# Optimization experiments

Hardware: AMD Instinct MI355X
Metric: run time of the kernel (lower is better)

## Reference

```python
import jax, jax.numpy as jnp
import numpy as np

N_NODES = 50000
N_EDGES = 800000
IN_F = 256
HEADS = 4
C = 32  # out_features // heads = 128 // 4
OUT_F = HEADS * C
NEG_SLOPE = 0.2
BN_EPS = 1e-5


def setup_inputs() -> dict:
    key = jax.random.key(0)
    ks = jax.random.split(key, 6)
    x = jax.random.normal(ks[0], (N_NODES, IN_F), dtype=jnp.float32)
    edge_index = jax.random.randint(ks[1], (2, N_EDGES), 0, N_NODES, dtype=jnp.int64)
    W = jax.random.normal(ks[2], (IN_F, OUT_F), dtype=jnp.float32) * 0.05
    att_src = jax.random.normal(ks[3], (HEADS, C), dtype=jnp.float32) * 0.05
    att_dst = jax.random.normal(ks[4], (HEADS, C), dtype=jnp.float32) * 0.05
    bias = jnp.zeros((OUT_F,), dtype=jnp.float32)
    gamma = jnp.ones((OUT_F,), dtype=jnp.float32)
    beta = jnp.zeros((OUT_F,), dtype=jnp.float32)
    return {"x": x, "edge_index": edge_index, "W": W, "att_src": att_src,
            "att_dst": att_dst, "bias": bias, "gamma": gamma, "beta": beta}


def reference(x, edge_index, W, att_src, att_dst, bias, gamma, beta):
    N = x.shape[0]
    # PyG GATConv adds self-loops by default
    loops = jnp.arange(N, dtype=edge_index.dtype)
    src = jnp.concatenate([edge_index[0], loops])  # [E+N]
    dst = jnp.concatenate([edge_index[1], loops])  # [E+N]

    h = (x @ W).reshape(N, HEADS, C)               # [N, H, C]
    a_src = jnp.sum(h * att_src, axis=-1)          # [N, H]
    a_dst = jnp.sum(h * att_dst, axis=-1)          # [N, H]

    e = a_src[src] + a_dst[dst]                    # [E', H]
    e = jax.nn.leaky_relu(e, NEG_SLOPE)
    # segment softmax over destination neighborhoods (self-loops ensure no empty segments)
    e_max = jax.ops.segment_max(e, dst, num_segments=N)
    e = jnp.exp(e - e_max[dst])
    denom = jax.ops.segment_sum(e, dst, num_segments=N)
    alpha = e / (denom[dst] + 1e-16)               # [E', H]

    msg = h[src] * alpha[:, :, None]               # [E', H, C]
    out = jax.ops.segment_sum(msg, dst, num_segments=N).reshape(N, OUT_F) + bias

    # BatchNorm1d in training mode (batch statistics, biased variance)
    mean = jnp.mean(out, axis=0)
    var = jnp.var(out, axis=0)
    out = (out - mean) * jax.lax.rsqrt(var + BN_EPS) * gamma + beta
    # ELU; dropout is identity in eval / deterministic reference
    return jax.nn.elu(out)
```

## Files before the change

kernel.cpp:

```cpp
#include <hip/hip_runtime.h>
#include <hip/hip_fp16.h>
#include <math.h>

#define NN 50000
#define EE 800000
#define EP (EE + NN)
#define INF_ 256
#define OF 128
#define NEG_SLOPE 0.2f
#define BN_EPS 1e-5f
#define NB 196
#define NWIN 8
#define DPW 6250
#define NCH 32
#define QPC 6250

typedef _Float16 half8 __attribute__((ext_vector_type(8)));
typedef float floatx4 __attribute__((ext_vector_type(4)));
typedef int intx4 __attribute__((ext_vector_type(4)));

__device__ __forceinline__ float lrelu_exp(float v) {
    v = v > 0.f ? v : NEG_SLOPE * v;
    return expf(v);
}

__global__ __launch_bounds__(256) void k_wprep(const float* __restrict__ W, _Float16* __restrict__ wfrag,
                                               float* __restrict__ fsum)
{
    int idx = blockIdx.x * 256 + threadIdx.x;
    if (idx < 256) fsum[idx] = 0.f;
    int j   = idx & 7;
    int l   = (idx >> 3) & 63;
    int t   = (idx >> 9) & 7;
    int ksg = idx >> 12;
    int k   = ksg * 32 + ((l >> 4) << 3) + j;
    int col = t * 16 + (l & 15);
    wfrag[idx] = (_Float16)W[k * OF + col];
}

__global__ __launch_bounds__(256) void k_gemm(
    const float* __restrict__ x, const _Float16* __restrict__ wfrag,
    const float* __restrict__ att_s, const float* __restrict__ att_d,
    _Float16* __restrict__ h, float* __restrict__ a_src, float* __restrict__ a_dst)
{
    __shared__ __align__(16) _Float16 smem[8192];
    _Float16* xh = smem;

    const int tid  = threadIdx.x;
    const int l    = tid & 63;
    const int w    = tid >> 6;
    const int row0 = blockIdx.x * 64;
    const int lrow = l & 15;
    const int lk8  = (l >> 4) << 3;

    floatx4 acc[8];
    #pragma unroll
    for (int t = 0; t < 8; ++t) acc[t] = (floatx4){0.f, 0.f, 0.f, 0.f};

    for (int kc = 0; kc < 4; ++kc) {
        __syncthreads();
        #pragma unroll
        for (int it = 0; it < 4; ++it) {
            int i  = tid + (it << 8);
            int r  = i >> 4;
            int c4 = (i & 15) << 2;
            int rr = row0 + r; if (rr >= NN) rr = NN - 1;
            float4 v = *(const float4*)&x[rr * INF_ + (kc << 6) + c4];
            _Float16* p = &xh[r * 72 + c4];
            p[0] = (_Float16)v.x; p[1] = (_Float16)v.y;
            p[2] = (_Float16)v.z; p[3] = (_Float16)v.w;
        }
        __syncthreads();
        #pragma unroll
        for (int ks = 0; ks < 2; ++ks) {
            int ksg = kc * 2 + ks;
            half8 a = *(half8*)&xh[(w * 16 + lrow) * 72 + (ks << 5) + lk8];
            const _Float16* wf = &wfrag[(ksg << 12) + (l << 3)];
            #pragma unroll
            for (int t = 0; t < 8; ++t) {
                half8 b = *(const half8*)&wf[t << 9];
                acc[t] = __builtin_amdgcn_mfma_f32_16x16x32_f16(a, b, acc[t], 0, 0, 0);
            }
        }
    }

    float as_c[8], ad_c[8];
    #pragma unroll
    for (int t = 0; t < 8; ++t) { as_c[t] = att_s[t * 16 + lrow]; ad_c[t] = att_d[t * 16 + lrow]; }
    float my_s = 0.f, my_d = 0.f;
    #pragma unroll
    for (int hh = 0; hh < 4; ++hh) {
        #pragma unroll
        for (int reg = 0; reg < 4; ++reg) {
            float ps = acc[2*hh][reg] * as_c[2*hh] + acc[2*hh+1][reg] * as_c[2*hh+1];
            float pd = acc[2*hh][reg] * ad_c[2*hh] + acc[2*hh+1][reg] * ad_c[2*hh+1];
            ps += __shfl_xor(ps, 1); ps += __shfl_xor(ps, 2); ps += __shfl_xor(ps, 4); ps += __shfl_xor(ps, 8);
            pd += __shfl_xor(pd, 1); pd += __shfl_xor(pd, 2); pd += __shfl_xor(pd, 4); pd += __shfl_xor(pd, 8);
            if (lrow == hh * 4 + reg) { my_s = ps; my_d = pd; }
        }
    }
    {
        int myreg = lrow & 3, myhh = lrow >> 2;
        int myrow = row0 + w * 16 + ((l >> 4) << 2) + myreg;
        if (myrow < NN) { a_src[myrow * 4 + myhh] = my_s; a_dst[myrow * 4 + myhh] = my_d; }
    }

    __syncthreads();
    _Float16* ldso = smem + w * 2048;
    #pragma unroll
    for (int t = 0; t < 8; ++t)
        #pragma unroll
        for (int reg = 0; reg < 4; ++reg)
            ldso[(((l >> 4) << 2) + reg) * 128 + t * 16 + lrow] = (_Float16)acc[t][reg];
    __syncthreads();
    {
        _Float16* gdst = h + (size_t)(row0 + w * 16) * OF;
        #pragma unroll
        for (int q = 0; q < 4; ++q) {
            int off = (q << 9) + (l << 3);
            *(half8*)&gdst[off] = *(half8*)&ldso[off];
        }
    }
}

__global__ __launch_bounds__(1024) void k_winhist(const int* __restrict__ ei, int* __restrict__ counts2)
{
    __shared__ int hist[DPW];
    const int w   = blockIdx.x & 7;
    const int c   = blockIdx.x >> 3;
    const int dlo = w * DPW;
    for (int i = threadIdx.x; i < DPW; i += 1024) hist[i] = 0;
    __syncthreads();
    const int q0 = c * QPC;
    for (int q = q0 + threadIdx.x; q < q0 + QPC; q += 1024) {
        intx4 d4 = __builtin_nontemporal_load(((const intx4*)(ei + EE)) + q);
        int dj[4] = {d4.x, d4.y, d4.z, d4.w};
        #pragma unroll
        for (int j = 0; j < 4; ++j) {
            unsigned d = (unsigned)(dj[j] - dlo);
            if (d < DPW) atomicAdd(&hist[d], 1);
        }
    }
    __syncthreads();
    int* dst = counts2 + c * NN + dlo;
    for (int i = threadIdx.x; i < DPW; i += 1024) dst[i] = hist[i];
}

__global__ __launch_bounds__(256) void k_blocksum(const int* __restrict__ counts2, int* __restrict__ partials)
{
    int i = blockIdx.x * 256 + threadIdx.x;
    int v = 0;
    if (i < NN) {
        v = 1;
        #pragma unroll 8
        for (int c = 0; c < NCH; ++c) v += counts2[c * NN + i];
    }
    v += __shfl_xor(v, 1);  v += __shfl_xor(v, 2);  v += __shfl_xor(v, 4);
    v += __shfl_xor(v, 8);  v += __shfl_xor(v, 16); v += __shfl_xor(v, 32);
    __shared__ int wsum[4];
    if ((threadIdx.x & 63) == 0) wsum[threadIdx.x >> 6] = v;
    __syncthreads();
    if (threadIdx.x == 0) partials[blockIdx.x] = wsum[0] + wsum[1] + wsum[2] + wsum[3];
}

__global__ __launch_bounds__(256) void k_writerows(
    const int* __restrict__ counts2, const int* __restrict__ partials,
    int* __restrict__ row_start, int* __restrict__ csr_src, int* __restrict__ base)
{
    __shared__ int smp[256];
    __shared__ int sm[256];
    int t = threadIdx.x;

    int pv = (t < NB) ? partials[t] : 0;
    smp[t] = pv;
    __syncthreads();
    for (int off = 1; off < 256; off <<= 1) {
        int u = (t >= off) ? smp[t - off] : 0;
        __syncthreads();
        smp[t] += u;
        __syncthreads();
    }
    int blockoff = (blockIdx.x > 0) ? smp[blockIdx.x - 1] : 0;

    int i = blockIdx.x * 256 + t;
    int v = 0;
    if (i < NN) {
        v = 1;
        #pragma unroll 8
        for (int c = 0; c < NCH; ++c) v += counts2[c * NN + i];
    }
    sm[t] = v;
    __syncthreads();
    for (int off = 1; off < 256; off <<= 1) {
        int u = (t >= off) ? sm[t - off] : 0;
        __syncthreads();
        sm[t] += u;
        __syncthreads();
    }
    int excl = blockoff + sm[t] - v;
    if (i < NN) {
        row_start[i] = excl;
        csr_src[excl] = i;
        int p = excl + 1;
        #pragma unroll 8
        for (int c = 0; c < NCH; ++c) { base[c * NN + i] = p; p += counts2[c * NN + i]; }
    }
    if (i == NN) row_start[NN] = excl;
}

__global__ __launch_bounds__(1024) void k_winfill(
    const int* __restrict__ ei, const int* __restrict__ base, int* __restrict__ csr_src)
{
    __shared__ int pos[DPW];
    const int w   = blockIdx.x & 7;
    const int c   = blockIdx.x >> 3;
    const int dlo = w * DPW;
    for (int i = threadIdx.x; i < DPW; i += 1024) pos[i] = base[c * NN + dlo + i];
    __syncthreads();
    const int q0 = c * QPC;
    for (int q = q0 + threadIdx.x; q < q0 + QPC; q += 1024) {
        intx4 d4 = __builtin_nontemporal_load(((const intx4*)(ei + EE)) + q);
        int idx0 = q << 2;
        int dj[4] = {d4.x, d4.y, d4.z, d4.w};
        #pragma unroll
        for (int j = 0; j < 4; ++j) {
            unsigned d = (unsigned)(dj[j] - dlo);
            if (d < DPW) {
                int p = atomicAdd(&pos[d], 1);
                csr_src[p] = ei[idx0 + j];
            }
        }
    }
}

__global__ __launch_bounds__(256) void k_gather(
    const _Float16* __restrict__ h, const int* __restrict__ csr_src,
    const int* __restrict__ row_start, const float* __restrict__ a_src,
    const float* __restrict__ a_dst, const float* __restrict__ bias,
    _Float16* __restrict__ outh)
{
    int node = blockIdx.x * 4 + (threadIdx.x >> 6);
    int lane = threadIdx.x & 63;
    int g    = lane >> 4;
    int c    = lane & 15;
    int head = c >> 2;
    int b = row_start[node];
    int e = row_start[node + 1];
    float ad = a_dst[(node << 2) + head];

    float acc[8] = {};
    float dsum = 0.f;
    int k = b;
    for (; k + 4 < e; k += 8) {
        int  kk0 = k + g;
        int  kk1 = k + 4 + g;
        bool act1 = kk1 < e;
        int  kc1 = act1 ? kk1 : b;
        int  s0  = csr_src[kk0];
        int  s1  = csr_src[kc1];
        float av0 = a_src[(s0 << 2) + head];
        float av1 = a_src[(s1 << 2) + head];
        half8 hv0 = *(const half8*)&h[(size_t)s0 * OF + (c << 3)];
        half8 hv1 = *(const half8*)&h[(size_t)s1 * OF + (c << 3)];
        float a0 = lrelu_exp(av0 + ad);
        float a1 = lrelu_exp(av1 + ad);
        if (!act1) a1 = 0.f;
        dsum += a0;
        #pragma unroll
        for (int j = 0; j < 8; ++j)
            acc[j] = fmaf(a0, (float)hv0[j], acc[j]);
        dsum += a1;
        #pragma unroll
        for (int j = 0; j < 8; ++j)
            acc[j] = fmaf(a1, (float)hv1[j], acc[j]);
    }
    for (; k < e; k += 4) {
        int  kk  = k + g;
        bool act = kk < e;
        int  kc  = act ? kk : b;
        int  s   = csr_src[kc];
        float a  = lrelu_exp(a_src[(s << 2) + head] + ad);
        if (!act) a = 0.f;
        dsum += a;
        half8 hv = *(const half8*)&h[(size_t)s * OF + (c << 3)];
        #pragma unroll
        for (int j = 0; j < 8; ++j)
            acc[j] = fmaf(a, (float)hv[j], acc[j]);
    }
    #pragma unroll
    for (int j = 0; j < 8; ++j) {
        acc[j] += __shfl_xor(acc[j], 16);
        acc[j] += __shfl_xor(acc[j], 32);
    }
    dsum += __shfl_xor(dsum, 16);
    dsum += __shfl_xor(dsum, 32);
    if (g == 0) {
        float inv = 1.0f / (dsum + 1e-16f);
        float4 b0 = *(const float4*)&bias[c << 3];
        float4 b1 = *(const float4*)&bias[(c << 3) + 4];
        float bj[8] = {b0.x, b0.y, b0.z, b0.w, b1.x, b1.y, b1.z, b1.w};
        half8 o;
        #pragma unroll
        for (int j = 0; j < 8; ++j)
            o[j] = (_Float16)fmaf(acc[j], inv, bj[j]);
        *(half8*)&outh[(size_t)node * OF + (c << 3)] = o;
    }
}

__global__ __launch_bounds__(256) void k_bnred(
    const _Float16* __restrict__ outh, float* __restrict__ fsum, float* __restrict__ fsumsq)
{
    int f = threadIdx.x & 127;
    int r = blockIdx.x * 2 + (threadIdx.x >> 7);
    float s = 0.f, ss = 0.f;
    for (; r < NN; r += gridDim.x * 2) {
        float v = (float)outh[r * OF + f];
        s += v;
        ss = fmaf(v, v, ss);
    }
    atomicAdd(&fsum[f], s);
    atomicAdd(&fsumsq[f], ss);
}

__global__ __launch_bounds__(256) void k_apply(
    const _Float16* __restrict__ outh, const float* __restrict__ fsum,
    const float* __restrict__ fsumsq, const float* __restrict__ gamma,
    const float* __restrict__ beta, float* __restrict__ out)
{
    __shared__ float ssc[128], ssh[128];
    if (threadIdx.x < 128) {
        int f = threadIdx.x;
        float mean = fsum[f] * (1.0f / NN);
        float var  = fsumsq[f] * (1.0f / NN) - mean * mean;
        float sc   = gamma[f] * rsqrtf(var + BN_EPS);
        ssc[f] = sc;
        ssh[f] = beta[f] - mean * sc;
    }
    __syncthreads();
    int i    = blockIdx.x * 256 + threadIdx.x;
    int base = i << 3;
    int f    = base & 127;
    half8 v  = *(const half8*)&outh[base];
    float r[8];
    #pragma unroll
    for (int j = 0; j < 8; ++j) {
        float t = fmaf((float)v[j], ssc[f + j], ssh[f + j]);
        r[j] = t > 0.f ? t : expm1f(t);
    }
    *(float4*)&out[base]     = make_float4(r[0], r[1], r[2], r[3]);
    *(float4*)&out[base + 4] = make_float4(r[4], r[5], r[6], r[7]);
}

extern "C" void kernel_launch(void* const* d_in, const int* in_sizes, int n_in,
                              void* d_out, int out_size, void* d_ws, size_t ws_size,
                              hipStream_t stream)
{
    const float* x     = (const float*)d_in[0];
    const int*   ei    = (const int*)d_in[1];
    const float* W     = (const float*)d_in[2];
    const float* att_s = (const float*)d_in[3];
    const float* att_d = (const float*)d_in[4];
    const float* bias  = (const float*)d_in[5];
    const float* gamma = (const float*)d_in[6];
    const float* beta  = (const float*)d_in[7];
    float* out = (float*)d_out;

    float* ws           = (float*)d_ws;
    _Float16* h         = (_Float16*)ws;
    _Float16* outh      = (_Float16*)(ws + 3210000);
    float* a_src        = ws + 6410000;
    float* a_dst        = a_src + 200000;
    float* wfrag_f      = a_dst + 200000;
    float* scratch_f    = wfrag_f + 20000;
    float* fsum         = scratch_f + 1700000;
    float* fsumsq       = fsum + 128;
    int* row_start      = (int*)(fsumsq + 128);
    int* csr_src        = row_start + NN + 1;
    int* partials       = csr_src + EP;
    int* counts2        = (int*)scratch_f;
    int* cbase          = (int*)outh;
    _Float16* wfrag     = (_Float16*)wfrag_f;

    k_wprep<<<128, 256, 0, stream>>>(W, wfrag, fsum);
    k_gemm<<<(NN + 63) / 64, 256, 0, stream>>>(x, wfrag, att_s, att_d, h, a_src, a_dst);
    k_winhist<<<NWIN * NCH, 1024, 0, stream>>>(ei, counts2);
    k_blocksum<<<NB, 256, 0, stream>>>(counts2, partials);
    k_writerows<<<NB, 256, 0, stream>>>(counts2, partials, row_start, csr_src, cbase);
    k_winfill<<<NWIN * NCH, 1024, 0, stream>>>(ei, cbase, csr_src);
    k_gather<<<NN / 4, 256, 0, stream>>>(h, csr_src, row_start, a_src, a_dst, bias, outh);
    k_bnred<<<512, 256, 0, stream>>>(outh, fsum, fsumsq);
    k_apply<<<NN * OF / 8 / 256, 256, 0, stream>>>(outh, fsum, fsumsq, gamma, beta, out);
}
```

Before: 150.9 us.

## Fold block-sum into histogram kernel, double edge chunks, reorder GEMM after CSR build

The separate block-sum kernel is removed. The histogram kernel now reduces its shared histogram per 256-node block and atomically adds the result into partials, which k_wprep preinitialises with the self-loop counts. The edge chunk count doubles to 64, giving more histogram and fill blocks, so 512 are launched. counts2 now reuses the h buffer, which is why the GEMM moves after the CSR build. The GEMM's LDS store is also vectorised to half4. The cost is a longer counts2 loop in writerows and more global atomics.

```diff
diff --git a/kernel.cpp b/kernel.cpp
--- a/kernel.cpp
+++ b/kernel.cpp
@@ -12,10 +12,11 @@
 #define NB 196
 #define NWIN 8
 #define DPW 6250
-#define NCH 32
-#define QPC 6250
+#define NCH 64
+#define QPC 3125
 
 typedef _Float16 half8 __attribute__((ext_vector_type(8)));
+typedef _Float16 half4 __attribute__((ext_vector_type(4)));
 typedef float floatx4 __attribute__((ext_vector_type(4)));
 typedef int intx4 __attribute__((ext_vector_type(4)));
 
@@ -25,10 +26,11 @@
 }
 
 __global__ __launch_bounds__(256) void k_wprep(const float* __restrict__ W, _Float16* __restrict__ wfrag,
-                                               float* __restrict__ fsum)
+                                               float* __restrict__ fsum, int* __restrict__ partials)
 {
     int idx = blockIdx.x * 256 + threadIdx.x;
     if (idx < 256) fsum[idx] = 0.f;
+    if (idx < NB) partials[idx] = (idx == NB - 1) ? (NN - (NB - 1) * 256) : 256;
     int j   = idx & 7;
     int l   = (idx >> 3) & 63;
     int t   = (idx >> 9) & 7;
@@ -38,6 +40,112 @@
     wfrag[idx] = (_Float16)W[k * OF + col];
 }
 
+__global__ __launch_bounds__(1024) void k_winhist(const int* __restrict__ ei, int* __restrict__ counts2,
+                                                  int* __restrict__ partials)
+{
+    __shared__ int hist[DPW];
+    const int w   = blockIdx.x & 7;
+    const int c   = blockIdx.x >> 3;
+    const int dlo = w * DPW;
+    for (int i = threadIdx.x; i < DPW; i += 1024) hist[i] = 0;
+    __syncthreads();
+    const int q0 = c * QPC;
+    for (int q = q0 + threadIdx.x; q < q0 + QPC; q += 1024) {
+        intx4 d4 = __builtin_nontemporal_load(((const intx4*)(ei + EE)) + q);
+        int dj[4] = {d4.x, d4.y, d4.z, d4.w};
+        #pragma unroll
+        for (int j = 0; j < 4; ++j) {
+            unsigned d = (unsigned)(dj[j] - dlo);
+            if (d < DPW) atomicAdd(&hist[d], 1);
+        }
+    }
+    __syncthreads();
+    int* dst = counts2 + c * NN + dlo;
+    for (int i = threadIdx.x; i < DPW; i += 1024) dst[i] = hist[i];
+    const int p0 = dlo >> 8;
+    const int p1 = (dlo + DPW - 1) >> 8;
+    int wid = threadIdx.x >> 6, lane = threadIdx.x & 63;
+    for (int p = p0 + wid; p <= p1; p += 16) {
+        int lo = p << 8;       if (lo < dlo)        lo = dlo;
+        int hi = (p + 1) << 8; if (hi > dlo + DPW)  hi = dlo + DPW;
+        int s = 0;
+        for (int i = lo - dlo + lane; i < hi - dlo; i += 64) s += hist[i];
+        s += __shfl_xor(s, 1);  s += __shfl_xor(s, 2);  s += __shfl_xor(s, 4);
+        s += __shfl_xor(s, 8);  s += __shfl_xor(s, 16); s += __shfl_xor(s, 32);
+        if (lane == 0 && s) atomicAdd(&partials[p], s);
+    }
+}
+
+__global__ __launch_bounds__(256) void k_writerows(
+    const int* __restrict__ counts2, const int* __restrict__ partials,
+    int* __restrict__ row_start, int* __restrict__ csr_src, int* __restrict__ base)
+{
+    __shared__ int smp[256];
+    __shared__ int sm[256];
+    int t = threadIdx.x;
+
+    int pv = (t < NB) ? partials[t] : 0;
+    smp[t] = pv;
+    __syncthreads();
+    for (int off = 1; off < 256; off <<= 1) {
+        int u = (t >= off) ? smp[t - off] : 0;
+        __syncthreads();
+        smp[t] += u;
+        __syncthreads();
+    }
+    int blockoff = (blockIdx.x > 0) ? smp[blockIdx.x - 1] : 0;
+
+    int i = blockIdx.x * 256 + t;
+    int v = 0;
+    if (i < NN) {
+        v = 1;
+        #pragma unroll 8
+        for (int c = 0; c < NCH; ++c) v += counts2[c * NN + i];
+    }
+    sm[t] = v;
+    __syncthreads();
+    for (int off = 1; off < 256; off <<= 1) {
+        int u = (t >= off) ? sm[t - off] : 0;
+        __syncthreads();
+        sm[t] += u;
+        __syncthreads();
+    }
+    int excl = blockoff + sm[t] - v;
+    if (i < NN) {
+        row_start[i] = excl;
+        csr_src[excl] = i;
+        int p = excl + 1;
+        #pragma unroll 8
+        for (int c = 0; c < NCH; ++c) { base[c * NN + i] = p; p += counts2[c * NN + i]; }
+    }
+    if (i == NN) row_start[NN] = excl;
+}
+
+__global__ __launch_bounds__(1024) void k_winfill(
+    const int* __restrict__ ei, const int* __restrict__ base, int* __restrict__ csr_src)
+{
+    __shared__ int pos[DPW];
+    const int w   = blockIdx.x & 7;
+    const int c   = blockIdx.x >> 3;
+    const int dlo = w * DPW;
+    for (int i = threadIdx.x; i < DPW; i += 1024) pos[i] = base[c * NN + dlo + i];
+    __syncthreads();
+    const int q0 = c * QPC;
+    for (int q = q0 + threadIdx.x; q < q0 + QPC; q += 1024) {
+        intx4 d4 = __builtin_nontemporal_load(((const intx4*)(ei + EE)) + q);
+        int idx0 = q << 2;
+        int dj[4] = {d4.x, d4.y, d4.z, d4.w};
+        #pragma unroll
+        for (int j = 0; j < 4; ++j) {
+            unsigned d = (unsigned)(dj[j] - dlo);
+            if (d < DPW) {
+                int p = atomicAdd(&pos[d], 1);
+                csr_src[p] = ei[idx0 + j];
+            }
+        }
+    }
+}
+
 __global__ __launch_bounds__(256) void k_gemm(
     const float* __restrict__ x, const _Float16* __restrict__ wfrag,
     const float* __restrict__ att_s, const float* __restrict__ att_d,
@@ -66,9 +174,10 @@
             int c4 = (i & 15) << 2;
             int rr = row0 + r; if (rr >= NN) rr = NN - 1;
             float4 v = *(const float4*)&x[rr * INF_ + (kc << 6) + c4];
-            _Float16* p = &xh[r * 72 + c4];
-            p[0] = (_Float16)v.x; p[1] = (_Float16)v.y;
-            p[2] = (_Float16)v.z; p[3] = (_Float16)v.w;
+            half4 hv;
+            hv[0] = (_Float16)v.x; hv[1] = (_Float16)v.y;
+            hv[2] = (_Float16)v.z; hv[3] = (_Float16)v.w;
+            *(half4*)&xh[r * 72 + c4] = hv;
         }
         __syncthreads();
         #pragma unroll
@@ -123,116 +232,6 @@
     }
 }
 
-__global__ __launch_bounds__(1024) void k_winhist(const int* __restrict__ ei, int* __restrict__ counts2)
-{
-    __shared__ int hist[DPW];
-    const int w   = blockIdx.x & 7;
-    const int c   = blockIdx.x >> 3;
-    const int dlo = w * DPW;
-    for (int i = threadIdx.x; i < DPW; i += 1024) hist[i] = 0;
-    __syncthreads();
-    const int q0 = c * QPC;
-    for (int q = q0 + threadIdx.x; q < q0 + QPC; q += 1024) {
-        intx4 d4 = __builtin_nontemporal_load(((const intx4*)(ei + EE)) + q);
-        int dj[4] = {d4.x, d4.y, d4.z, d4.w};
-        #pragma unroll
-        for (int j = 0; j < 4; ++j) {
-            unsigned d = (unsigned)(dj[j] - dlo);
-            if (d < DPW) atomicAdd(&hist[d], 1);
-        }
-    }
-    __syncthreads();
-    int* dst = counts2 + c * NN + dlo;
-    for (int i = threadIdx.x; i < DPW; i += 1024) dst[i] = hist[i];
-}
-
-__global__ __launch_bounds__(256) void k_blocksum(const int* __restrict__ counts2, int* __restrict__ partials)
-{
-    int i = blockIdx.x * 256 + threadIdx.x;
-    int v = 0;
-    if (i < NN) {
-        v = 1;
-        #pragma unroll 8
-        for (int c = 0; c < NCH; ++c) v += counts2[c * NN + i];
-    }
-    v += __shfl_xor(v, 1);  v += __shfl_xor(v, 2);  v += __shfl_xor(v, 4);
-    v += __shfl_xor(v, 8);  v += __shfl_xor(v, 16); v += __shfl_xor(v, 32);
-    __shared__ int wsum[4];
-    if ((threadIdx.x & 63) == 0) wsum[threadIdx.x >> 6] = v;
-    __syncthreads();
-    if (threadIdx.x == 0) partials[blockIdx.x] = wsum[0] + wsum[1] + wsum[2] + wsum[3];
-}
-
-__global__ __launch_bounds__(256) void k_writerows(
-    const int* __restrict__ counts2, const int* __restrict__ partials,
-    int* __restrict__ row_start, int* __restrict__ csr_src, int* __restrict__ base)
-{
-    __shared__ int smp[256];
-    __shared__ int sm[256];
-    int t = threadIdx.x;
-
-    int pv = (t < NB) ? partials[t] : 0;
-    smp[t] = pv;
-    __syncthreads();
-    for (int off = 1; off < 256; off <<= 1) {
-        int u = (t >= off) ? smp[t - off] : 0;
-        __syncthreads();
-        smp[t] += u;
-        __syncthreads();
-    }
-    int blockoff = (blockIdx.x > 0) ? smp[blockIdx.x - 1] : 0;
-
-    int i = blockIdx.x * 256 + t;
-    int v = 0;
-    if (i < NN) {
-        v = 1;
-        #pragma unroll 8
-        for (int c = 0; c < NCH; ++c) v += counts2[c * NN + i];
-    }
-    sm[t] = v;
-    __syncthreads();
-    for (int off = 1; off < 256; off <<= 1) {
-        int u = (t >= off) ? sm[t - off] : 0;
-        __syncthreads();
-        sm[t] += u;
-        __syncthreads();
-    }
-    int excl = blockoff + sm[t] - v;
-    if (i < NN) {
-        row_start[i] = excl;
-        csr_src[excl] = i;
-        int p = excl + 1;
-        #pragma unroll 8
-        for (int c = 0; c < NCH; ++c) { base[c * NN + i] = p; p += counts2[c * NN + i]; }
-    }
-    if (i == NN) row_start[NN] = excl;
-}
-
-__global__ __launch_bounds__(1024) void k_winfill(
-    const int* __restrict__ ei, const int* __restrict__ base, int* __restrict__ csr_src)
-{
-    __shared__ int pos[DPW];
-    const int w   = blockIdx.x & 7;
-    const int c   = blockIdx.x >> 3;
-    const int dlo = w * DPW;
-    for (int i = threadIdx.x; i < DPW; i += 1024) pos[i] = base[c * NN + dlo + i];
-    __syncthreads();
-    const int q0 = c * QPC;
-    for (int q = q0 + threadIdx.x; q < q0 + QPC; q += 1024) {
-        intx4 d4 = __builtin_nontemporal_load(((const intx4*)(ei + EE)) + q);
-        int idx0 = q << 2;
-        int dj[4] = {d4.x, d4.y, d4.z, d4.w};
-        #pragma unroll
-        for (int j = 0; j < 4; ++j) {
-            unsigned d = (unsigned)(dj[j] - dlo);
-            if (d < DPW) {
-                int p = atomicAdd(&pos[d], 1);
-                csr_src[p] = ei[idx0 + j];
-            }
-        }
-    }
-}
-
 __global__ __launch_bounds__(256) void k_gather(
     const _Float16* __restrict__ h, const int* __restrict__ csr_src,
     const int* __restrict__ row_start, const float* __restrict__ a_src,
@@ -252,11 +251,10 @@
     float dsum = 0.f;
     int k = b;
     for (; k + 4 < e; k += 8) {
-        int  kk0 = k + g;
         int  kk1 = k + 4 + g;
         bool act1 = kk1 < e;
         int  kc1 = act1 ? kk1 : b;
-        int  s0  = csr_src[kk0];
+        int  s0  = csr_src[k + g];
         int  s1  = csr_src[kc1];
         float av0 = a_src[(s0 << 2) + head];
         float av1 = a_src[(s1 << 2) + head];
@@ -371,22 +369,20 @@
     float* a_src        = ws + 6410000;
     float* a_dst        = a_src + 200000;
     float* wfrag_f      = a_dst + 200000;
-    float* scratch_f    = wfrag_f + 20000;
-    float* fsum         = scratch_f + 1700000;
+    float* fsum         = wfrag_f + 20000;
     float* fsumsq       = fsum + 128;
     int* row_start      = (int*)(fsumsq + 128);
     int* csr_src        = row_start + NN + 1;
     int* partials       = csr_src + EP;
-    int* counts2        = (int*)scratch_f;
+    int* counts2        = (int*)h;
     int* cbase          = (int*)outh;
     _Float16* wfrag     = (_Float16*)wfrag_f;
 
-    k_wprep<<<128, 256, 0, stream>>>(W, wfrag, fsum);
-    k_gemm<<<(NN + 63) / 64, 256, 0, stream>>>(x, wfrag, att_s, att_d, h, a_src, a_dst);
-    k_winhist<<<NWIN * NCH, 1024, 0, stream>>>(ei, counts2);
-    k_blocksum<<<NB, 256, 0, stream>>>(counts2, partials);
+    k_wprep<<<128, 256, 0, stream>>>(W, wfrag, fsum, partials);
+    k_winhist<<<NWIN * NCH, 1024, 0, stream>>>(ei, counts2, partials);
     k_writerows<<<NB, 256, 0, stream>>>(counts2, partials, row_start, csr_src, cbase);
     k_winfill<<<NWIN * NCH, 1024, 0, stream>>>(ei, cbase, csr_src);
+    k_gemm<<<(NN + 63) / 64, 256, 0, stream>>>(x, wfrag, att_s, att_d, h, a_src, a_dst);
     k_gather<<<NN / 4, 256, 0, stream>>>(h, csr_src, row_start, a_src, a_dst, bias, outh);
     k_bnred<<<512, 256, 0, stream>>>(outh, fsum, fsumsq);
     k_apply<<<NN * OF / 8 / 256, 256, 0, stream>>>(outh, fsum, fsumsq, gamma, beta, out);
```

Measured after the change: 175.0 us. 1.16x slower.
